# Kernel tuning notes

Measured on AMD Instinct MI355X. Metric: run time of the kernel, lower is better.

## Reference

```python
import jax, jax.numpy as jnp
import numpy as np

B, C_IN, C_OUT, IMG, K_STEPS = 32, 64, 8, 128, 8


def setup_inputs() -> dict:
    key = jax.random.key(0)
    k1, k2, k3, k4, k5 = jax.random.split(key, 5)
    x = jax.random.normal(k1, (B, C_IN, IMG, IMG), dtype=jnp.float32)
    rand_pixel = jax.random.uniform(k2, (B, 1, IMG, IMG), dtype=jnp.float32)
    conv_w = jax.random.normal(k3, (C_OUT, C_IN), dtype=jnp.float32) * (1.0 / np.sqrt(C_IN))
    conv_b = jax.random.normal(k4, (C_OUT,), dtype=jnp.float32) * 0.01
    gate = jax.random.normal(k5, (), dtype=jnp.float32)
    # gaussian kernel init: sigma = 1 / (K_steps * log 2)
    log_sigma = jnp.asarray(np.log(1.0 / (K_STEPS * np.log(2.0))), dtype=jnp.float32)
    return {"x": x, "rand_pixel": rand_pixel, "conv_w": conv_w, "conv_b": conv_b,
            "gate": gate, "log_sigma": log_sigma}


def _semiconv(x, conv_w, conv_b, gate):
    # 1x1 conv == channel contraction
    out = gate * (jnp.einsum('oc,bchw->bohw', conv_w, x) + conv_b[None, :, None, None])
    B_, Cout, H, W = out.shape
    g1, g2 = jnp.meshgrid(jnp.linspace(-1.0, 1.0, H), jnp.linspace(-1.0, 1.0, W), indexing='ij')
    coords = jnp.stack([g1, g2])[None].astype(out.dtype)          # [1,2,H,W]
    uv = jnp.concatenate([jnp.zeros((1, Cout - 2, H, W), out.dtype), coords], axis=1)
    return out + uv


def reference(x, rand_pixel, conv_w, conv_b, gate, log_sigma):
    Bsz, _, H, W = x.shape
    feat = _semiconv(x, conv_w, conv_b, gate)              # [B,Cout,H,W]
    Cout = feat.shape[1]
    feat_flat = feat.reshape(Bsz, Cout, H * W)
    sigma = jnp.exp(log_sigma)

    def step(log_scope, _):
        # seed pixel selection: argmax of rand * scope over image
        pixel_probs = rand_pixel * jnp.exp(log_scope)       # [B,1,H,W]
        flat_idx = jnp.argmax(pixel_probs.reshape(Bsz, -1), axis=1)   # [B]
        seed = jnp.take_along_axis(feat_flat, flat_idx[:, None, None], axis=2)  # [B,Cout,1]
        sq_dist = jnp.sum((feat_flat - seed) ** 2, axis=1).reshape(Bsz, 1, H, W)
        alpha = jnp.exp(-sq_dist / sigma)                   # gaussian kernel
        # straight-through clamp to [0.01, 0.99]
        alpha = alpha + jax.lax.stop_gradient(jnp.clip(alpha, 0.01, 0.99) - alpha)
        log_m = log_scope + jnp.log(alpha)
        new_scope = log_scope + jnp.log1p(-alpha)
        return new_scope, (log_m, new_scope)

    log_scope0 = jnp.zeros((Bsz, 1, H, W), feat.dtype)
    final_scope, (lms, lss) = jax.lax.scan(step, log_scope0, None, length=K_STEPS - 1)
    # lms/lss: [K-1,B,1,H,W]
    log_masks = jnp.concatenate([lms, final_scope[None]], axis=0)   # last mask = final scope
    log_scopes = jnp.concatenate([log_scope0[None], lss], axis=0)
    log_masks = jnp.moveaxis(log_masks[:, :, 0], 0, 1)    # [B,K,H,W]
    log_scopes = jnp.moveaxis(log_scopes[:, :, 0], 0, 1)  # [B,K,H,W]
    return log_masks, log_scopes
```

## Files before the change

### kernel.cpp

```cpp
#include <hip/hip_runtime.h>

#define C_IN 64
#define C_OUT 8
#define IMG 128
#define HW (IMG * IMG)
#define BATCH 32
#define K_STEPS 8

#define FEAT_BYTES ((size_t)BATCH * HW * C_OUT * 4)
#define BLK_PER_B 8
#define NFLAGS ((K_STEPS - 1) * BATCH * BLK_PER_B)

__global__ __launch_bounds__(256) void semiconv_kernel(
    const float* __restrict__ x,
    const float* __restrict__ w,
    const float* __restrict__ bias,
    const float* __restrict__ gate_p,
    float* __restrict__ feat,
    unsigned long long* __restrict__ flags)
{
    __shared__ float sw[C_OUT * C_IN];
    const int tid = threadIdx.x;
    if (blockIdx.x == 0) {
        for (int k = tid; k < NFLAGS; k += 256) flags[k] = 0ULL;
    }
    for (int i = tid; i < C_OUT * C_IN; i += 256) sw[i] = w[i];
    __syncthreads();

    const int b  = blockIdx.x >> 4;
    const int p4 = (((blockIdx.x & 15) * 256) + tid) * 4;

    const float gate = *gate_p;
    const float* xb = x + (long long)b * C_IN * HW + p4;

    float acc[C_OUT][4];
    #pragma unroll
    for (int o = 0; o < C_OUT; ++o) {
        const float bv = bias[o];
        #pragma unroll
        for (int j = 0; j < 4; ++j) acc[o][j] = bv;
    }

    for (int c = 0; c < C_IN; ++c) {
        const float4 xv = *(const float4*)(xb + c * HW);
        const float xs[4] = {xv.x, xv.y, xv.z, xv.w};
        #pragma unroll
        for (int o = 0; o < C_OUT; ++o) {
            const float wv = sw[o * C_IN + c];
            #pragma unroll
            for (int j = 0; j < 4; ++j) acc[o][j] = fmaf(wv, xs[j], acc[o][j]);
        }
    }

    const int row  = p4 / IMG;
    const int col0 = p4 % IMG;
    const float step = 2.0f / (IMG - 1);
    const float g1 = -1.0f + step * (float)row;

    float* dst = feat + ((long long)b * HW + p4) * C_OUT;
    #pragma unroll
    for (int j = 0; j < 4; ++j) {
        float o0 = gate * acc[0][j];
        float o1 = gate * acc[1][j];
        float o2 = gate * acc[2][j];
        float o3 = gate * acc[3][j];
        float o4 = gate * acc[4][j];
        float o5 = gate * acc[5][j];
        float o6 = gate * acc[6][j] + g1;
        float o7 = gate * acc[7][j] + (-1.0f + step * (float)(col0 + j));
        *(float4*)(dst + j * C_OUT)     = make_float4(o0, o1, o2, o3);
        *(float4*)(dst + j * C_OUT + 4) = make_float4(o4, o5, o6, o7);
    }
}

#define NT 1024
#define CHUNK (HW / BLK_PER_B)

__global__ __launch_bounds__(NT) void stick_kernel(
    const float* __restrict__ feat,
    const float* __restrict__ rand_pixel,
    const float* __restrict__ log_sigma_p,
    float* __restrict__ masks,
    float* __restrict__ scopes,
    unsigned long long* __restrict__ flags)
{
    const int b    = blockIdx.x & 31;
    const int blk  = blockIdx.x >> 5;
    const int tid  = threadIdx.x;
    const int lane = tid & 63;
    const int wid  = tid >> 6;

    const float inv_sigma = expf(-(*log_sigma_p));

    const float* fb = feat + (size_t)b * HW * C_OUT;
    const float* rb = rand_pixel + (size_t)b * HW;
    float* mb = masks  + (size_t)b * (K_STEPS * HW);
    float* sb = scopes + (size_t)b * (K_STEPS * HW);

    const int p0 = blk * CHUNK + 2 * tid;

    const float4 f0a = *(const float4*)(fb + (size_t)p0 * C_OUT);
    const float4 f0b = *(const float4*)(fb + (size_t)p0 * C_OUT + 4);
    const float4 f1a = *(const float4*)(fb + (size_t)p0 * C_OUT + 8);
    const float4 f1b = *(const float4*)(fb + (size_t)p0 * C_OUT + 12);

    const float2 rr = *(const float2*)(rb + p0);
    float ls0 = 0.0f, ls1 = 0.0f;
    *(float2*)(sb + p0) = make_float2(0.0f, 0.0f);

    __shared__ float swv[2][16];
    __shared__ int   swi[2][16];

    for (int s = 0; s < K_STEPS - 1; ++s) {
        const int par = s & 1;
        const int recbase = (s * BATCH + b) * BLK_PER_B;

        float bv; int bi;
        {
            const float v0 = rr.x * expf(ls0);
            const float v1 = rr.y * expf(ls1);
            bv = v0; bi = p0;
            if (v1 > bv) { bv = v1; bi = p0 + 1; }
        }
        #pragma unroll
        for (int off = 1; off < 64; off <<= 1) {
            const float ov = __shfl_xor(bv, off);
            const int   oi = __shfl_xor(bi, off);
            if (ov > bv || (ov == bv && oi < bi)) { bv = ov; bi = oi; }
        }
        if (lane == 0) { swv[par][wid] = bv; swi[par][wid] = bi; }
        __syncthreads();

        float cv = (lane < 16) ? swv[par][lane] : -1.0f;
        int   ci = (lane < 16) ? swi[par][lane] : 0x7fffffff;
        #pragma unroll
        for (int off = 1; off < 16; off <<= 1) {
            const float ov = __shfl_xor(cv, off);
            const int   oi = __shfl_xor(ci, off);
            if (ov > cv || (ov == cv && oi < ci)) { cv = ov; ci = oi; }
        }
        if (wid == 0 && lane == 0) {
            const unsigned long long pk =
                ((unsigned long long)__float_as_uint(cv) << 32) |
                (unsigned long long)(unsigned int)(ci + 1);
            __hip_atomic_store(&flags[recbase + blk], pk,
                               __ATOMIC_RELAXED, __HIP_MEMORY_SCOPE_AGENT);
        }
        float gv = -1.0f; int gi = 0x7fffffff;
        if (lane < BLK_PER_B) {
            unsigned long long got;
            do {
                got = __hip_atomic_load(&flags[recbase + lane],
                                        __ATOMIC_RELAXED,
                                        __HIP_MEMORY_SCOPE_AGENT);
            } while (got == 0ULL);
            gv = __uint_as_float((unsigned int)(got >> 32));
            gi = (int)(unsigned int)(got & 0xffffffffULL) - 1;
        }
        #pragma unroll
        for (int off = 1; off < 8; off <<= 1) {
            const float ov = __shfl_xor(gv, off);
            const int   oi = __shfl_xor(gi, off);
            if (ov > gv || (ov == gv && oi < gi)) { gv = ov; gi = oi; }
        }
        const int seedIdx = __shfl(gi, 0);

        const float4 s0 = *(const float4*)(fb + (size_t)seedIdx * C_OUT);
        const float4 s1 = *(const float4*)(fb + (size_t)seedIdx * C_OUT + 4);

        float sq0 = 0.0f, sq1 = 0.0f, d;
        d = f0a.x - s0.x; sq0 += d * d;
        d = f0a.y - s0.y; sq0 += d * d;
        d = f0a.z - s0.z; sq0 += d * d;
        d = f0a.w - s0.w; sq0 += d * d;
        d = f0b.x - s1.x; sq0 += d * d;
        d = f0b.y - s1.y; sq0 += d * d;
        d = f0b.z - s1.z; sq0 += d * d;
        d = f0b.w - s1.w; sq0 += d * d;
        d = f1a.x - s0.x; sq1 += d * d;
        d = f1a.y - s0.y; sq1 += d * d;
        d = f1a.z - s0.z; sq1 += d * d;
        d = f1a.w - s0.w; sq1 += d * d;
        d = f1b.x - s1.x; sq1 += d * d;
        d = f1b.y - s1.y; sq1 += d * d;
        d = f1b.z - s1.z; sq1 += d * d;
        d = f1b.w - s1.w; sq1 += d * d;

        float m0, m1;
        {
            const float t = sq0 * inv_sigma;
            float alpha = expf(-t);
            float log_a;
            if (alpha >= 0.99f)      { alpha = 0.99f; log_a = -0.010050336f; }
            else if (alpha <= 0.01f) { alpha = 0.01f; log_a = -4.6051702f;  }
            else                     { log_a = -t; }
            m0 = ls0 + log_a;
            ls0 += log1pf(-alpha);
        }
        {
            const float t = sq1 * inv_sigma;
            float alpha = expf(-t);
            float log_a;
            if (alpha >= 0.99f)      { alpha = 0.99f; log_a = -0.010050336f; }
            else if (alpha <= 0.01f) { alpha = 0.01f; log_a = -4.6051702f;  }
            else                     { log_a = -t; }
            m1 = ls1 + log_a;
            ls1 += log1pf(-alpha);
        }
        *(float2*)(mb + s * HW + p0)       = make_float2(m0, m1);
        *(float2*)(sb + (s + 1) * HW + p0) = make_float2(ls0, ls1);
    }

    *(float2*)(mb + (K_STEPS - 1) * HW + p0) = make_float2(ls0, ls1);
}

extern "C" void kernel_launch(void* const* d_in, const int* in_sizes, int n_in,
                              void* d_out, int out_size, void* d_ws, size_t ws_size,
                              hipStream_t stream) {
    const float* x          = (const float*)d_in[0];
    const float* rand_pixel = (const float*)d_in[1];
    const float* conv_w     = (const float*)d_in[2];
    const float* conv_b     = (const float*)d_in[3];
    const float* gate       = (const float*)d_in[4];
    const float* log_sigma  = (const float*)d_in[5];

    float* masks  = (float*)d_out;
    float* scopes = masks + (long long)BATCH * K_STEPS * HW;

    float* feat = (float*)d_ws;
    unsigned long long* flags =
        (unsigned long long*)((char*)d_ws + FEAT_BYTES);

    semiconv_kernel<<<(BATCH * HW) / (256 * 4), 256, 0, stream>>>(
        x, conv_w, conv_b, gate, feat, flags);

    stick_kernel<<<BATCH * BLK_PER_B, NT, 0, stream>>>(
        feat, rand_pixel, log_sigma, masks, scopes, flags);
}
```

Measured before the change: 77.80 us.

## Precompute first-step seed argmax in conv kernel, narrow grid sync to one wave, nontemporal stores

The first seed's argmax uses scope zero, so it now depends only on rand_pixel. The conv kernel computes per-block partial argmaxes for it, which removes the cross-block flag exchange for step 0 in the stick kernel. For later steps, only wave 0 does the block-level reduction and flag polling, and the result is broadcast through shared memory with an extra barrier. Mask and scope outputs are written with nontemporal stores to limit cache pollution. The cost is extra work and a rand_pixel read in the conv kernel, plus one more __syncthreads per step.

```diff
diff --git a/kernel.cpp b/kernel.cpp
--- a/kernel.cpp
+++ b/kernel.cpp
@@ -10,16 +10,23 @@
 #define FEAT_BYTES ((size_t)BATCH * HW * C_OUT * 4)
 #define BLK_PER_B 8
 #define NFLAGS ((K_STEPS - 1) * BATCH * BLK_PER_B)
+#define NSEED0 (BATCH * 16)
+
+union F2U { float2 f2; unsigned long long u; };
 
 __global__ __launch_bounds__(256) void semiconv_kernel(
     const float* __restrict__ x,
     const float* __restrict__ w,
     const float* __restrict__ bias,
     const float* __restrict__ gate_p,
+    const float* __restrict__ rand_pixel,
     float* __restrict__ feat,
-    unsigned long long* __restrict__ flags)
+    unsigned long long* __restrict__ flags,
+    unsigned long long* __restrict__ seed0)
 {
     __shared__ float sw[C_OUT * C_IN];
+    __shared__ float spv[4];
+    __shared__ int   spi[4];
     const int tid = threadIdx.x;
     if (blockIdx.x == 0) {
         for (int k = tid; k < NFLAGS; k += 256) flags[k] = 0ULL;
@@ -27,8 +34,9 @@
     for (int i = tid; i < C_OUT * C_IN; i += 256) sw[i] = w[i];
     __syncthreads();
 
-    const int b  = blockIdx.x >> 4;
-    const int p4 = (((blockIdx.x & 15) * 256) + tid) * 4;
+    const int b     = blockIdx.x >> 4;
+    const int blk16 = blockIdx.x & 15;
+    const int p4    = ((blk16 * 256) + tid) * 4;
 
     const float gate = *gate_p;
     const float* xb = x + (long long)b * C_IN * HW + p4;
@@ -71,10 +79,41 @@
         *(float4*)(dst + j * C_OUT)     = make_float4(o0, o1, o2, o3);
         *(float4*)(dst + j * C_OUT + 4) = make_float4(o4, o5, o6, o7);
     }
+
+    const int lane = tid & 63;
+    const int wid  = tid >> 6;
+    const float4 rv = *(const float4*)(rand_pixel + (size_t)b * HW + p4);
+    float bv = rv.x; int bi = p4;
+    if (rv.y > bv) { bv = rv.y; bi = p4 + 1; }
+    if (rv.z > bv) { bv = rv.z; bi = p4 + 2; }
+    if (rv.w > bv) { bv = rv.w; bi = p4 + 3; }
+    #pragma unroll
+    for (int off = 1; off < 64; off <<= 1) {
+        const float ov = __shfl_xor(bv, off);
+        const int   oi = __shfl_xor(bi, off);
+        if (ov > bv || (ov == bv && oi < bi)) { bv = ov; bi = oi; }
+    }
+    if (lane == 0) { spv[wid] = bv; spi[wid] = bi; }
+    __syncthreads();
+    if (tid == 0) {
+        float v = spv[0]; int ix = spi[0];
+        #pragma unroll
+        for (int wv2 = 1; wv2 < 4; ++wv2) {
+            if (spv[wv2] > v || (spv[wv2] == v && spi[wv2] < ix)) { v = spv[wv2]; ix = spi[wv2]; }
+        }
+        seed0[(b << 4) | blk16] =
+            ((unsigned long long)__float_as_uint(v) << 32) |
+            (unsigned long long)(unsigned int)ix;
+    }
 }
 
 #define NT 1024
 #define CHUNK (HW / BLK_PER_B)
+
+__device__ __forceinline__ void nt_store2(float* p, float a, float bfl) {
+    F2U v; v.f2 = make_float2(a, bfl);
+    __builtin_nontemporal_store(v.u, (unsigned long long*)p);
+}
 
 __global__ __launch_bounds__(NT) void stick_kernel(
     const float* __restrict__ feat,
@@ -82,7 +121,8 @@
     const float* __restrict__ log_sigma_p,
     float* __restrict__ masks,
     float* __restrict__ scopes,
-    unsigned long long* __restrict__ flags)
+    unsigned long long* __restrict__ flags,
+    const unsigned long long* __restrict__ seed0)
 {
     const int b    = blockIdx.x & 31;
     const int blk  = blockIdx.x >> 5;
@@ -106,64 +146,87 @@
 
     const float2 rr = *(const float2*)(rb + p0);
     float ls0 = 0.0f, ls1 = 0.0f;
-    *(float2*)(sb + p0) = make_float2(0.0f, 0.0f);
+    nt_store2(sb + p0, 0.0f, 0.0f);
 
     __shared__ float swv[2][16];
     __shared__ int   swi[2][16];
+    __shared__ int   sSeed[2];
 
     for (int s = 0; s < K_STEPS - 1; ++s) {
         const int par = s & 1;
-        const int recbase = (s * BATCH + b) * BLK_PER_B;
-
-        float bv; int bi;
-        {
-            const float v0 = rr.x * expf(ls0);
-            const float v1 = rr.y * expf(ls1);
-            bv = v0; bi = p0;
-            if (v1 > bv) { bv = v1; bi = p0 + 1; }
-        }
-        #pragma unroll
-        for (int off = 1; off < 64; off <<= 1) {
-            const float ov = __shfl_xor(bv, off);
-            const int   oi = __shfl_xor(bi, off);
-            if (ov > bv || (ov == bv && oi < bi)) { bv = ov; bi = oi; }
-        }
-        if (lane == 0) { swv[par][wid] = bv; swi[par][wid] = bi; }
-        __syncthreads();
-
-        float cv = (lane < 16) ? swv[par][lane] : -1.0f;
-        int   ci = (lane < 16) ? swi[par][lane] : 0x7fffffff;
-        #pragma unroll
-        for (int off = 1; off < 16; off <<= 1) {
-            const float ov = __shfl_xor(cv, off);
-            const int   oi = __shfl_xor(ci, off);
-            if (ov > cv || (ov == cv && oi < ci)) { cv = ov; ci = oi; }
-        }
-        if (wid == 0 && lane == 0) {
-            const unsigned long long pk =
-                ((unsigned long long)__float_as_uint(cv) << 32) |
-                (unsigned long long)(unsigned int)(ci + 1);
-            __hip_atomic_store(&flags[recbase + blk], pk,
-                               __ATOMIC_RELAXED, __HIP_MEMORY_SCOPE_AGENT);
-        }
-        float gv = -1.0f; int gi = 0x7fffffff;
-        if (lane < BLK_PER_B) {
-            unsigned long long got;
-            do {
-                got = __hip_atomic_load(&flags[recbase + lane],
-                                        __ATOMIC_RELAXED,
-                                        __HIP_MEMORY_SCOPE_AGENT);
-            } while (got == 0ULL);
-            gv = __uint_as_float((unsigned int)(got >> 32));
-            gi = (int)(unsigned int)(got & 0xffffffffULL) - 1;
-        }
-        #pragma unroll
-        for (int off = 1; off < 8; off <<= 1) {
-            const float ov = __shfl_xor(gv, off);
-            const int   oi = __shfl_xor(gi, off);
-            if (ov > gv || (ov == gv && oi < gi)) { gv = ov; gi = oi; }
-        }
-        const int seedIdx = __shfl(gi, 0);
+        int seedIdx;
+
+        if (s == 0) {
+            float gv = -1.0f; int gi = 0x7fffffff;
+            if (lane < 16) {
+                const unsigned long long got = seed0[(b << 4) | lane];
+                gv = __uint_as_float((unsigned int)(got >> 32));
+                gi = (int)(unsigned int)(got & 0xffffffffULL);
+            }
+            #pragma unroll
+            for (int off = 1; off < 16; off <<= 1) {
+                const float ov = __shfl_xor(gv, off);
+                const int   oi = __shfl_xor(gi, off);
+                if (ov > gv || (ov == gv && oi < gi)) { gv = ov; gi = oi; }
+            }
+            seedIdx = __shfl(gi, 0);
+        } else {
+            const int recbase = (s * BATCH + b) * BLK_PER_B;
+
+            float bv; int bi;
+            {
+                const float v0 = rr.x * expf(ls0);
+                const float v1 = rr.y * expf(ls1);
+                bv = v0; bi = p0;
+                if (v1 > bv) { bv = v1; bi = p0 + 1; }
+            }
+            #pragma unroll
+            for (int off = 1; off < 64; off <<= 1) {
+                const float ov = __shfl_xor(bv, off);
+                const int   oi = __shfl_xor(bi, off);
+                if (ov > bv || (ov == bv && oi < bi)) { bv = ov; bi = oi; }
+            }
+            if (lane == 0) { swv[par][wid] = bv; swi[par][wid] = bi; }
+            __syncthreads();
+
+            if (wid == 0) {
+                float v = (lane < 16) ? swv[par][lane] : -1.0f;
+                int   ix = (lane < 16) ? swi[par][lane] : 0x7fffffff;
+                #pragma unroll
+                for (int off = 1; off < 16; off <<= 1) {
+                    const float ov = __shfl_xor(v, off);
+                    const int   oi = __shfl_xor(ix, off);
+                    if (ov > v || (ov == v && oi < ix)) { v = ov; ix = oi; }
+                }
+                if (lane == 0) {
+                    const unsigned long long pk =
+                        ((unsigned long long)__float_as_uint(v) << 32) |
+                        (unsigned long long)(unsigned int)(ix + 1);
+                    __hip_atomic_store(&flags[recbase + blk], pk,
+                                       __ATOMIC_RELAXED, __HIP_MEMORY_SCOPE_AGENT);
+                }
+                float gv = -1.0f; int gi = 0x7fffffff;
+                if (lane < BLK_PER_B) {
+                    unsigned long long got;
+                    do {
+                        got = __hip_atomic_load(&flags[recbase + lane],
+                                                __ATOMIC_RELAXED,
+                                                __HIP_MEMORY_SCOPE_AGENT);
+                    } while (got == 0ULL);
+                    gv = __uint_as_float((unsigned int)(got >> 32));
+                    gi = (int)(unsigned int)(got & 0xffffffffULL) - 1;
+                }
+                #pragma unroll
+                for (int off = 1; off < 8; off <<= 1) {
+                    const float ov = __shfl_xor(gv, off);
+                    const int   oi = __shfl_xor(gi, off);
+                    if (ov > gv || (ov == gv && oi < gi)) { gv = ov; gi = oi; }
+                }
+                if (lane == 0) sSeed[par] = gi;
+            }
+            __syncthreads();
+            seedIdx = sSeed[par];
+        }
 
         const float4 s0 = *(const float4*)(fb + (size_t)seedIdx * C_OUT);
         const float4 s1 = *(const float4*)(fb + (size_t)seedIdx * C_OUT + 4);
@@ -207,11 +270,11 @@
             m1 = ls1 + log_a;
             ls1 += log1pf(-alpha);
         }
-        *(float2*)(mb + s * HW + p0)       = make_float2(m0, m1);
-        *(float2*)(sb + (s + 1) * HW + p0) = make_float2(ls0, ls1);
-    }
-
-    *(float2*)(mb + (K_STEPS - 1) * HW + p0) = make_float2(ls0, ls1);
+        nt_store2(mb + s * HW + p0, m0, m1);
+        nt_store2(sb + (s + 1) * HW + p0, ls0, ls1);
+    }
+
+    nt_store2(mb + (K_STEPS - 1) * HW + p0, ls0, ls1);
 }
 
 extern "C" void kernel_launch(void* const* d_in, const int* in_sizes, int n_in,
@@ -230,10 +293,11 @@
     float* feat = (float*)d_ws;
     unsigned long long* flags =
         (unsigned long long*)((char*)d_ws + FEAT_BYTES);
+    unsigned long long* seed0 = flags + NFLAGS;
 
     semiconv_kernel<<<(BATCH * HW) / (256 * 4), 256, 0, stream>>>(
-        x, conv_w, conv_b, gate, feat, flags);
+        x, conv_w, conv_b, gate, rand_pixel, feat, flags, seed0);
 
     stick_kernel<<<BATCH * BLK_PER_B, NT, 0, stream>>>(
-        feat, rand_pixel, log_sigma, masks, scopes, flags);
+        feat, rand_pixel, log_sigma, masks, scopes, flags, seed0);
 }
```

After: 72.64 us. 6.6% less time.
